# Kernel optimization log

Measured on AMD Instinct MI355X. Metric: run time of the kernel, lower is better.

The kernel has to match this reference:

```python
import jax, jax.numpy as jnp
import numpy as np

B, N, C, E = 8, 4096, 128, 131072  # batch, nodes, channels (in==out), edges


def _linear_params(key, fan_in, fan_out):
    kw, kb = jax.random.split(key)
    s = 1.0 / np.sqrt(fan_in).astype(np.float32)
    W = jax.random.uniform(kw, (fan_in, fan_out), jnp.float32, -s, s)
    b = jax.random.uniform(kb, (fan_out,), jnp.float32, -s, s)
    return W, b


def setup_inputs() -> dict:
    key = jax.random.key(0)
    ks = jax.random.split(key, 6)
    x = jax.random.normal(ks[0], (B, N, C), jnp.float32)
    edge_index = jax.random.randint(ks[1], (2, E), 0, N, jnp.int64)
    W0, b0 = _linear_params(ks[2], C, C)        # lin0: in -> out
    W1, b1 = _linear_params(ks[3], 2 * C, C)    # lin1: 2*out -> out
    W2, b2 = _linear_params(ks[4], C, C)        # lin2: out -> out
    Wo, bo = _linear_params(ks[5], C, C)        # output: out -> out
    return {"x": x, "edge_index": edge_index, "W0": W0, "b0": b0,
            "W1": W1, "b1": b1, "W2": W2, "b2": b2, "Wo": Wo, "bo": bo}


def reference(x, edge_index, W0, b0, W1, b1, W2, b2, Wo, bo):
    n = x.shape[1]
    # symmetric 0/1 adjacency (duplicate edges collapse via .set), zero diagonal
    adj = jnp.zeros((n, n), x.dtype)
    adj = adj.at[edge_index[0], edge_index[1]].set(1.0)
    adj = adj.at[edge_index[1], edge_index[0]].set(1.0)
    diag = jnp.arange(n)
    adj = adj.at[diag, diag].set(0.0)
    h = x @ W0 + b0                               # [B, N, C]
    agg = jnp.einsum('ij,bjd->bid', adj, h)       # neighbor aggregation
    cat = jnp.concatenate([x, agg], axis=-1)      # [B, N, 2C]
    out = (cat @ W1 + b1) @ W2 + b2
    out = jax.nn.gelu(out, approximate=False) @ Wo + bo  # torch exact GELU
    return x + out
```

## Files before the change

### kernel.cpp

```cpp
#include <hip/hip_runtime.h>
#include <hip/hip_bf16.h>
#include <math.h>

#define NN 4096
#define BB 8
#define CC 128
#define EE 131072
#define M_ROWS (BB*NN)
#define DEG_CAP 512

typedef __attribute__((ext_vector_type(8))) short short8;
typedef __attribute__((ext_vector_type(4))) float f32x4;

__device__ __forceinline__ float bf2f(unsigned int u){
    union { unsigned int i; float f; } v; v.i = u << 16; return v.f;
}
__device__ __forceinline__ unsigned short f2bf(float f){
    union { float f; unsigned int i; } v; v.f = f;
    unsigned int u = v.i;
    unsigned int r = u + 0x7FFFu + ((u >> 16) & 1u);
    return (unsigned short)(r >> 16);
}

__device__ __forceinline__ int swz(int r, int k2 ){
    return r * 256 + (k2 ^ ((r & 7) << 4));
}

__global__ __launch_bounds__(256) void k_init(uint4* __restrict__ bits4,
                                              const float* __restrict__ W0, const float* __restrict__ W1,
                                              const float* __restrict__ W2, const float* __restrict__ Wo,
                                              unsigned short* __restrict__ Wt0, unsigned short* __restrict__ Wt1a,
                                              unsigned short* __restrict__ Wt1b, unsigned short* __restrict__ Wt2,
                                              unsigned short* __restrict__ Wto){
    int bid = blockIdx.x, t = threadIdx.x;
    if (bid < 512){
        bits4[bid * 256 + t] = (uint4){0u, 0u, 0u, 0u};
        return;
    }
    int idx = (bid - 512) * 256 + t;
    int s = idx >> 14;
    int e = idx & 16383;
    int n = e >> 7, k = e & 127;
    float v; unsigned short* dst;
    switch (s){
        case 0:  v = W0[k*128+n];        dst = Wt0;  break;
        case 1:  v = W1[k*128+n];        dst = Wt1a; break;
        case 2:  v = W1[(128+k)*128+n];  dst = Wt1b; break;
        case 3:  v = W2[k*128+n];        dst = Wt2;  break;
        default: v = Wo[k*128+n];        dst = Wto;  break;
    }
    dst[n*128+k] = f2bf(v);
}

__global__ __launch_bounds__(256) void k_scatter(const int* __restrict__ ei,
                                                 unsigned int* __restrict__ bits){
    int e = blockIdx.x * blockDim.x + threadIdx.x;
    if (e < EE){
        int u = ei[e], v = ei[EE + e];
        atomicOr(&bits[u * 128 + (v >> 5)], 1u << (v & 31));
        atomicOr(&bits[v * 128 + (u >> 5)], 1u << (u & 31));
    }
}

__global__ __launch_bounds__(128) void k_csr(const unsigned int* __restrict__ bits,
                                             int* __restrict__ cols, int* __restrict__ deg){
    __shared__ int sc[128];
    int i = blockIdx.x, t = threadIdx.x;
    unsigned int w = bits[i * 128 + t];
    if (t == (i >> 5)) w &= ~(1u << (i & 31));
    int c = __popc(w);
    sc[t] = c; __syncthreads();
    int val = c;
    for (int off = 1; off < 128; off <<= 1){
        int add = (t >= off) ? sc[t - off] : 0;
        __syncthreads();
        val += add; sc[t] = val;
        __syncthreads();
    }
    int total = sc[127];
    int pos = val - c;
    unsigned int ww = w;
    while (ww){
        int b = __ffs(ww) - 1;
        ww &= ww - 1;
        if (pos < DEG_CAP) cols[(size_t)i * DEG_CAP + pos] = t * 32 + b;
        pos++;
    }
    if (t == 0) deg[i] = total < DEG_CAP ? total : DEG_CAP;
}

__device__ __forceinline__ void acc8u(uint4 u, float* a){
    a[0] += bf2f(u.x & 0xFFFFu); a[1] += bf2f(u.x >> 16);
    a[2] += bf2f(u.y & 0xFFFFu); a[3] += bf2f(u.y >> 16);
    a[4] += bf2f(u.z & 0xFFFFu); a[5] += bf2f(u.z >> 16);
    a[6] += bf2f(u.w & 0xFFFFu); a[7] += bf2f(u.w >> 16);
}

__global__ __launch_bounds__(256) void k_agg(const unsigned short* __restrict__ h,
                                             const int* __restrict__ cols,
                                             const int* __restrict__ deg,
                                             unsigned short* __restrict__ agg){
    __shared__ int scol[4][DEG_CAP];
    const int t = threadIdx.x;
    const int w = t >> 6, lane = t & 63;
    const int sub = lane >> 4, li = lane & 15;
    const int b = blockIdx.x & 7;
    const int i = ((blockIdx.x >> 3) << 2) + w;
    const int d = deg[i];
    const int* cl = cols + (size_t)i * DEG_CAP;
    for (int q = lane; q < d; q += 64) scol[w][q] = cl[q];

    const unsigned short* hb = h + (size_t)b * (NN*128) + li * 8;
    float a[8];
    #pragma unroll
    for (int c = 0; c < 8; c++) a[c] = 0.f;

    int n = sub;
    for (; n + 4 < d; n += 8){
        int j0 = scol[w][n], j1 = scol[w][n+4];
        uint4 u0 = *((const uint4*)(hb + ((size_t)j0 << 7)));
        uint4 u1 = *((const uint4*)(hb + ((size_t)j1 << 7)));
        acc8u(u0, a); acc8u(u1, a);
    }
    if (n < d){
        uint4 u0 = *((const uint4*)(hb + ((size_t)scol[w][n] << 7)));
        acc8u(u0, a);
    }

    #pragma unroll
    for (int c = 0; c < 8; c++){
        a[c] += __shfl_xor(a[c], 16);
        a[c] += __shfl_xor(a[c], 32);
    }
    if (sub == 0){
        uint4 o;
        o.x = (unsigned)f2bf(a[0]) | ((unsigned)f2bf(a[1]) << 16);
        o.y = (unsigned)f2bf(a[2]) | ((unsigned)f2bf(a[3]) << 16);
        o.z = (unsigned)f2bf(a[4]) | ((unsigned)f2bf(a[5]) << 16);
        o.w = (unsigned)f2bf(a[6]) | ((unsigned)f2bf(a[7]) << 16);
        *((uint4*)(agg + (size_t)b * (NN*128) + ((size_t)i << 7) + li * 8)) = o;
    }
}

__device__ __forceinline__ void stage_a_bf16(const unsigned short* __restrict__ src, int blockRow,
                                             unsigned short* As, int t){
    #pragma unroll
    for (int it = 0; it < 4; ++it){
        int g = it * 2048 + t * 8;
        int r = g >> 7, k = g & 127;
        uint4 v = *((const uint4*)(src + (size_t)(blockRow + r) * 128 + k));
        *((uint4*)((char*)As + swz(r, k * 2))) = v;
    }
}
__device__ __forceinline__ void stage_a_f32(const float* __restrict__ src, int blockRow,
                                            unsigned short* As, int t){
    #pragma unroll
    for (int it = 0; it < 4; ++it){
        int g = it * 2048 + t * 8;
        int r = g >> 7, k = g & 127;
        const float* p = src + (size_t)(blockRow + r) * 128 + k;
        float4 lo = *((const float4*)p);
        float4 hi = *((const float4*)(p + 4));
        ushort4 w0, w1;
        w0.x = f2bf(lo.x); w0.y = f2bf(lo.y); w0.z = f2bf(lo.z); w0.w = f2bf(lo.w);
        w1.x = f2bf(hi.x); w1.y = f2bf(hi.y); w1.z = f2bf(hi.z); w1.w = f2bf(hi.w);
        char* dst = (char*)As + swz(r, k * 2);
        *((ushort4*)dst) = w0;
        *((ushort4*)(dst + 8)) = w1;
    }
}
__device__ __forceinline__ void stage_w(const unsigned short* __restrict__ Wt,
                                        unsigned short* Ws, int t){
    #pragma unroll
    for (int it = 0; it < 8; ++it){
        int g = it * 2048 + t * 8;
        int r = g >> 7, k = g & 127;
        uint4 v = *((const uint4*)(Wt + r * 128 + k));
        *((uint4*)((char*)Ws + swz(r, k * 2))) = v;
    }
}
__device__ __forceinline__ void mfma_pass(const unsigned short* As, const unsigned short* Ws,
                                          int wr, int wc, int l15, int lh, f32x4 acc[2][4]){
    #pragma unroll
    for (int ks = 0; ks < 4; ++ks){
        const int kc = ks * 32 + lh * 8;
        short8 af[2], bfv[4];
        #pragma unroll
        for (int m = 0; m < 2; m++){
            int r = wr + m * 16 + l15;
            af[m] = *((const short8*)((const char*)As + swz(r, kc * 2)));
        }
        #pragma unroll
        for (int n = 0; n < 4; n++){
            int r = wc + n * 16 + l15;
            bfv[n] = *((const short8*)((const char*)Ws + swz(r, kc * 2)));
        }
        #pragma unroll
        for (int m = 0; m < 2; m++)
            #pragma unroll
            for (int n = 0; n < 4; n++)
                acc[m][n] = __builtin_amdgcn_mfma_f32_16x16x32_bf16(af[m], bfv[n], acc[m][n], 0, 0, 0);
    }
}

__global__ __launch_bounds__(256) void k_gemm0(const float* __restrict__ x,
                                               const unsigned short* __restrict__ Wt0,
                                               const float* __restrict__ b0,
                                               unsigned short* __restrict__ h){
    __shared__ unsigned short As[64*128];
    __shared__ unsigned short Ws[128*128];
    const int t = threadIdx.x;
    const int blockRow = blockIdx.x * 64;
    stage_a_f32(x, blockRow, As, t);
    stage_w(Wt0, Ws, t);
    __syncthreads();
    const int lane = t & 63, w = t >> 6;
    const int wr = (w >> 1) * 32, wc = (w & 1) * 64;
    const int l15 = lane & 15, lh = lane >> 4;
    f32x4 acc[2][4];
    #pragma unroll
    for (int m = 0; m < 2; m++) for (int n = 0; n < 4; n++) acc[m][n] = (f32x4)(0.0f);
    mfma_pass(As, Ws, wr, wc, l15, lh, acc);
    #pragma unroll
    for (int m = 0; m < 2; m++){
        #pragma unroll
        for (int rr = 0; rr < 4; rr++){
            int row = blockRow + wr + m * 16 + lh * 4 + rr;
            #pragma unroll
            for (int n = 0; n < 4; n++){
                int col = wc + n * 16 + l15;
                float v = acc[m][n][rr] + b0[col];
                h[(size_t)row * 128 + col] = f2bf(v);
            }
        }
    }
}

__global__ __launch_bounds__(256) void k_gemm1(const float* __restrict__ x,
                                               const unsigned short* __restrict__ agg,
                                               const unsigned short* __restrict__ Wt1a,
                                               const unsigned short* __restrict__ Wt1b,
                                               const float* __restrict__ b1,
                                               unsigned short* __restrict__ t1bf){
    __shared__ unsigned short As[64*128];
    __shared__ unsigned short Ws[128*128];
    const int t = threadIdx.x;
    const int blockRow = blockIdx.x * 64;
    const int lane = t & 63, w = t >> 6;
    const int wr = (w >> 1) * 32, wc = (w & 1) * 64;
    const int l15 = lane & 15, lh = lane >> 4;
    f32x4 acc[2][4];
    #pragma unroll
    for (int m = 0; m < 2; m++) for (int n = 0; n < 4; n++) acc[m][n] = (f32x4)(0.0f);

    stage_a_f32(x, blockRow, As, t);
    stage_w(Wt1a, Ws, t);
    __syncthreads();
    mfma_pass(As, Ws, wr, wc, l15, lh, acc);
    __syncthreads();
    stage_a_bf16(agg, blockRow, As, t);
    stage_w(Wt1b, Ws, t);
    __syncthreads();
    mfma_pass(As, Ws, wr, wc, l15, lh, acc);

    #pragma unroll
    for (int m = 0; m < 2; m++){
        #pragma unroll
        for (int rr = 0; rr < 4; rr++){
            int row = blockRow + wr + m * 16 + lh * 4 + rr;
            #pragma unroll
            for (int n = 0; n < 4; n++){
                int col = wc + n * 16 + l15;
                float v = acc[m][n][rr] + b1[col];
                t1bf[(size_t)row * 128 + col] = f2bf(v);
            }
        }
    }
}

__global__ __launch_bounds__(256) void k_gemm23(const unsigned short* __restrict__ t1bf,
                                                const unsigned short* __restrict__ Wt2,
                                                const unsigned short* __restrict__ Wto,
                                                const float* __restrict__ b2,
                                                const float* __restrict__ bo,
                                                const float* __restrict__ x,
                                                float* __restrict__ out){
    __shared__ unsigned short As[64*128];
    __shared__ unsigned short Ws2[128*128];
    __shared__ unsigned short Wso[128*128];
    const int t = threadIdx.x;
    const int blockRow = blockIdx.x * 64;
    const int lane = t & 63, w = t >> 6;
    const int wr = (w >> 1) * 32, wc = (w & 1) * 64;
    const int l15 = lane & 15, lh = lane >> 4;

    stage_a_bf16(t1bf, blockRow, As, t);
    stage_w(Wt2, Ws2, t);
    stage_w(Wto, Wso, t);
    __syncthreads();

    f32x4 acc[2][4];
    #pragma unroll
    for (int m = 0; m < 2; m++) for (int n = 0; n < 4; n++) acc[m][n] = (f32x4)(0.0f);
    mfma_pass(As, Ws2, wr, wc, l15, lh, acc);
    __syncthreads();

    #pragma unroll
    for (int m = 0; m < 2; m++){
        #pragma unroll
        for (int rr = 0; rr < 4; rr++){
            int rl = wr + m * 16 + lh * 4 + rr;
            #pragma unroll
            for (int n = 0; n < 4; n++){
                int col = wc + n * 16 + l15;
                float v = acc[m][n][rr] + b2[col];
                v = 0.5f * v * (1.0f + erff(v * 0.70710678118f));
                *((unsigned short*)((char*)As + swz(rl, col * 2))) = f2bf(v);
            }
        }
    }
    __syncthreads();

    f32x4 acc2[2][4];
    #pragma unroll
    for (int m = 0; m < 2; m++) for (int n = 0; n < 4; n++) acc2[m][n] = (f32x4)(0.0f);
    mfma_pass(As, Wso, wr, wc, l15, lh, acc2);

    #pragma unroll
    for (int m = 0; m < 2; m++){
        #pragma unroll
        for (int rr = 0; rr < 4; rr++){
            int row = blockRow + wr + m * 16 + lh * 4 + rr;
            #pragma unroll
            for (int n = 0; n < 4; n++){
                int col = wc + n * 16 + l15;
                float v = acc2[m][n][rr] + bo[col] + x[(size_t)row * 128 + col];
                out[(size_t)row * 128 + col] = v;
            }
        }
    }
}

extern "C" void kernel_launch(void* const* d_in, const int* in_sizes, int n_in,
                              void* d_out, int out_size, void* d_ws, size_t ws_size,
                              hipStream_t stream) {
    const float* x  = (const float*)d_in[0];
    const int*   ei = (const int*)d_in[1];
    const float* W0 = (const float*)d_in[2];
    const float* b0 = (const float*)d_in[3];
    const float* W1 = (const float*)d_in[4];
    const float* b1 = (const float*)d_in[5];
    const float* W2 = (const float*)d_in[6];
    const float* b2 = (const float*)d_in[7];
    const float* Wo = (const float*)d_in[8];
    const float* bo = (const float*)d_in[9];
    float* out = (float*)d_out;

    char* ws = (char*)d_ws;
    unsigned int* bits   = (unsigned int*)(ws + 0);
    int*   cols          = (int*)(ws + 2097152);
    int*   deg           = (int*)(ws + 10485760);
    unsigned short* h    = (unsigned short*)(ws + 10502144);
    unsigned short* aggb = (unsigned short*)(ws + 18890752);
    unsigned short* t1bf = (unsigned short*)(ws + 27279360);
    unsigned short* Wt0  = (unsigned short*)(ws + 35667968);
    unsigned short* Wt1a = (unsigned short*)(ws + 35667968 + 32768);
    unsigned short* Wt1b = (unsigned short*)(ws + 35667968 + 65536);
    unsigned short* Wt2  = (unsigned short*)(ws + 35667968 + 98304);
    unsigned short* Wto  = (unsigned short*)(ws + 35667968 + 131072);

    k_init<<<832, 256, 0, stream>>>((uint4*)bits, W0, W1, W2, Wo, Wt0, Wt1a, Wt1b, Wt2, Wto);
    k_scatter<<<EE / 256, 256, 0, stream>>>(ei, bits);
    k_csr<<<NN, 128, 0, stream>>>(bits, cols, deg);

    k_gemm0<<<M_ROWS / 64, 256, 0, stream>>>(x, Wt0, b0, h);
    k_agg<<<BB * (NN / 4), 256, 0, stream>>>(h, cols, deg, aggb);
    k_gemm1<<<M_ROWS / 64, 256, 0, stream>>>(x, aggb, Wt1a, Wt1b, b1, t1bf);
    k_gemm23<<<M_ROWS / 64, 256, 0, stream>>>(t1bf, Wt2, Wto, b2, bo, x, out);
}
```

Baseline: 77.20 us.

## Reassociate aggregation to use raw x and fold W0 into W1b; fuse MLP

Uses linearity to aggregate the bf16 copy of x directly (adj·x), then applies the precomputed product W0·W1b, and adds a degree-scaled bias term (deg·b0·W1b). This removes the separate gemm0 pass and the h intermediate. All remaining GEMMs (lin1, lin2, GELU, output) are fused into one kernel that reuses shared memory. x is converted to bf16 once in the init kernel, and a single-block kernel computes the weight product and bias vector. Risks: the serial single-block k_wprod on the critical path, and some extra precision loss from rounding the composed weight to bf16.

```diff
diff --git a/kernel.cpp b/kernel.cpp
--- a/kernel.cpp
+++ b/kernel.cpp
@@ -27,27 +27,40 @@
 }
 
 __global__ __launch_bounds__(256) void k_init(uint4* __restrict__ bits4,
+                                              const float* __restrict__ x,
+                                              unsigned short* __restrict__ xb,
                                               const float* __restrict__ W0, const float* __restrict__ W1,
                                               const float* __restrict__ W2, const float* __restrict__ Wo,
-                                              unsigned short* __restrict__ Wt0, unsigned short* __restrict__ Wt1a,
-                                              unsigned short* __restrict__ Wt1b, unsigned short* __restrict__ Wt2,
-                                              unsigned short* __restrict__ Wto){
+                                              unsigned short* __restrict__ Wt1a, unsigned short* __restrict__ Wt1b,
+                                              unsigned short* __restrict__ Wt2,  unsigned short* __restrict__ Wto,
+                                              unsigned short* __restrict__ W0bf){
     int bid = blockIdx.x, t = threadIdx.x;
     if (bid < 512){
         bits4[bid * 256 + t] = (uint4){0u, 0u, 0u, 0u};
         return;
     }
-    int idx = (bid - 512) * 256 + t;
+    if (bid < 2560){
+        size_t e = (size_t)(bid - 512) * 2048 + t * 8;
+        float4 lo = *((const float4*)(x + e));
+        float4 hi = *((const float4*)(x + e + 4));
+        ushort4 w0, w1;
+        w0.x = f2bf(lo.x); w0.y = f2bf(lo.y); w0.z = f2bf(lo.z); w0.w = f2bf(lo.w);
+        w1.x = f2bf(hi.x); w1.y = f2bf(hi.y); w1.z = f2bf(hi.z); w1.w = f2bf(hi.w);
+        *((ushort4*)(xb + e)) = w0;
+        *((ushort4*)(xb + e + 4)) = w1;
+        return;
+    }
+    int idx = (bid - 2560) * 256 + t;
     int s = idx >> 14;
     int e = idx & 16383;
     int n = e >> 7, k = e & 127;
     float v; unsigned short* dst;
     switch (s){
-        case 0:  v = W0[k*128+n];        dst = Wt0;  break;
-        case 1:  v = W1[k*128+n];        dst = Wt1a; break;
-        case 2:  v = W1[(128+k)*128+n];  dst = Wt1b; break;
-        case 3:  v = W2[k*128+n];        dst = Wt2;  break;
-        default: v = Wo[k*128+n];        dst = Wto;  break;
+        case 0:  v = W1[k*128+n];        dst = Wt1a; break;
+        case 1:  v = W1[(128+k)*128+n];  dst = Wt1b; break;
+        case 2:  v = W2[k*128+n];        dst = Wt2;  break;
+        case 3:  v = Wo[k*128+n];        dst = Wto;  break;
+        default: v = W0[n*128+k];        dst = W0bf; break;
     }
     dst[n*128+k] = f2bf(v);
 }
@@ -89,6 +102,109 @@
     if (t == 0) deg[i] = total < DEG_CAP ? total : DEG_CAP;
 }
 
+__device__ __forceinline__ void stage_w(const unsigned short* __restrict__ Wt,
+                                        unsigned short* Ws, int t){
+    #pragma unroll
+    for (int it = 0; it < 8; ++it){
+        int g = it * 2048 + t * 8;
+        int r = g >> 7, k = g & 127;
+        uint4 v = *((const uint4*)(Wt + r * 128 + k));
+        *((uint4*)((char*)Ws + swz(r, k * 2))) = v;
+    }
+}
+__device__ __forceinline__ void stage_a_bf16(const unsigned short* __restrict__ src, int blockRow,
+                                             unsigned short* As, int t){
+    #pragma unroll
+    for (int it = 0; it < 4; ++it){
+        int g = it * 2048 + t * 8;
+        int r = g >> 7, k = g & 127;
+        uint4 v = *((const uint4*)(src + (size_t)(blockRow + r) * 128 + k));
+        *((uint4*)((char*)As + swz(r, k * 2))) = v;
+    }
+}
+__device__ __forceinline__ void mfma_pass(const unsigned short* As, const unsigned short* Ws,
+                                          int wr, int wc, int l15, int lh, f32x4 acc[2][4]){
+    #pragma unroll
+    for (int ks = 0; ks < 4; ++ks){
+        const int kc = ks * 32 + lh * 8;
+        short8 af[2], bfv[4];
+        #pragma unroll
+        for (int m = 0; m < 2; m++){
+            int r = wr + m * 16 + l15;
+            af[m] = *((const short8*)((const char*)As + swz(r, kc * 2)));
+        }
+        #pragma unroll
+        for (int n = 0; n < 4; n++){
+            int r = wc + n * 16 + l15;
+            bfv[n] = *((const short8*)((const char*)Ws + swz(r, kc * 2)));
+        }
+        #pragma unroll
+        for (int m = 0; m < 2; m++)
+            #pragma unroll
+            for (int n = 0; n < 4; n++)
+                acc[m][n] = __builtin_amdgcn_mfma_f32_16x16x32_bf16(af[m], bfv[n], acc[m][n], 0, 0, 0);
+    }
+}
+
+__global__ __launch_bounds__(256) void k_wprod(const unsigned short* __restrict__ W0bf,
+                                               const unsigned short* __restrict__ Wt1b,
+                                               const float* __restrict__ b0,
+                                               const float* __restrict__ W1,
+                                               unsigned short* __restrict__ Wtu,
+                                               float* __restrict__ c1){
+    __shared__ unsigned short As[128*128];
+    __shared__ unsigned short Ws[128*128];
+    const int t = threadIdx.x;
+    stage_w(W0bf, As, t);
+    stage_w(Wt1b, Ws, t);
+    __syncthreads();
+    const int lane = t & 63, w = t >> 6;
+    const int wr = w * 32;
+    const int l15 = lane & 15, lh = lane >> 4;
+    f32x4 acc[2][8];
+    #pragma unroll
+    for (int m = 0; m < 2; m++) for (int n = 0; n < 8; n++) acc[m][n] = (f32x4)(0.0f);
+    #pragma unroll
+    for (int ks = 0; ks < 4; ++ks){
+        const int kc = ks * 32 + lh * 8;
+        short8 af[2], bfv[8];
+        #pragma unroll
+        for (int m = 0; m < 2; m++){
+            int r = wr + m * 16 + l15;
+            af[m] = *((const short8*)((const char*)As + swz(r, kc * 2)));
+        }
+        #pragma unroll
+        for (int n = 0; n < 8; n++){
+            int r = n * 16 + l15;
+            bfv[n] = *((const short8*)((const char*)Ws + swz(r, kc * 2)));
+        }
+        #pragma unroll
+        for (int m = 0; m < 2; m++)
+            #pragma unroll
+            for (int n = 0; n < 8; n++)
+                acc[m][n] = __builtin_amdgcn_mfma_f32_16x16x32_bf16(af[m], bfv[n], acc[m][n], 0, 0, 0);
+    }
+    #pragma unroll
+    for (int m = 0; m < 2; m++){
+        #pragma unroll
+        for (int rr = 0; rr < 4; rr++){
+            int r = wr + m * 16 + lh * 4 + rr;
+            #pragma unroll
+            for (int n = 0; n < 8; n++){
+                int c = n * 16 + l15;
+                Wtu[c * 128 + r] = f2bf(acc[m][n][rr]);
+            }
+        }
+    }
+    if (t < 128){
+        float s = 0.f;
+        #pragma unroll 8
+        for (int k = 0; k < 128; k++)
+            s += b0[k] * W1[(size_t)(128 + k) * 128 + t];
+        c1[t] = s;
+    }
+}
+
 __device__ __forceinline__ void acc8u(uint4 u, float* a){
     a[0] += bf2f(u.x & 0xFFFFu); a[1] += bf2f(u.x >> 16);
     a[2] += bf2f(u.y & 0xFFFFu); a[3] += bf2f(u.y >> 16);
@@ -126,7 +242,6 @@
         uint4 u0 = *((const uint4*)(hb + ((size_t)scol[w][n] << 7)));
         acc8u(u0, a);
     }
-
     #pragma unroll
     for (int c = 0; c < 8; c++){
         a[c] += __shfl_xor(a[c], 16);
@@ -142,106 +257,19 @@
     }
 }
 
-__device__ __forceinline__ void stage_a_bf16(const unsigned short* __restrict__ src, int blockRow,
-                                             unsigned short* As, int t){
-    #pragma unroll
-    for (int it = 0; it < 4; ++it){
-        int g = it * 2048 + t * 8;
-        int r = g >> 7, k = g & 127;
-        uint4 v = *((const uint4*)(src + (size_t)(blockRow + r) * 128 + k));
-        *((uint4*)((char*)As + swz(r, k * 2))) = v;
-    }
-}
-__device__ __forceinline__ void stage_a_f32(const float* __restrict__ src, int blockRow,
-                                            unsigned short* As, int t){
-    #pragma unroll
-    for (int it = 0; it < 4; ++it){
-        int g = it * 2048 + t * 8;
-        int r = g >> 7, k = g & 127;
-        const float* p = src + (size_t)(blockRow + r) * 128 + k;
-        float4 lo = *((const float4*)p);
-        float4 hi = *((const float4*)(p + 4));
-        ushort4 w0, w1;
-        w0.x = f2bf(lo.x); w0.y = f2bf(lo.y); w0.z = f2bf(lo.z); w0.w = f2bf(lo.w);
-        w1.x = f2bf(hi.x); w1.y = f2bf(hi.y); w1.z = f2bf(hi.z); w1.w = f2bf(hi.w);
-        char* dst = (char*)As + swz(r, k * 2);
-        *((ushort4*)dst) = w0;
-        *((ushort4*)(dst + 8)) = w1;
-    }
-}
-__device__ __forceinline__ void stage_w(const unsigned short* __restrict__ Wt,
-                                        unsigned short* Ws, int t){
-    #pragma unroll
-    for (int it = 0; it < 8; ++it){
-        int g = it * 2048 + t * 8;
-        int r = g >> 7, k = g & 127;
-        uint4 v = *((const uint4*)(Wt + r * 128 + k));
-        *((uint4*)((char*)Ws + swz(r, k * 2))) = v;
-    }
-}
-__device__ __forceinline__ void mfma_pass(const unsigned short* As, const unsigned short* Ws,
-                                          int wr, int wc, int l15, int lh, f32x4 acc[2][4]){
-    #pragma unroll
-    for (int ks = 0; ks < 4; ++ks){
-        const int kc = ks * 32 + lh * 8;
-        short8 af[2], bfv[4];
-        #pragma unroll
-        for (int m = 0; m < 2; m++){
-            int r = wr + m * 16 + l15;
-            af[m] = *((const short8*)((const char*)As + swz(r, kc * 2)));
-        }
-        #pragma unroll
-        for (int n = 0; n < 4; n++){
-            int r = wc + n * 16 + l15;
-            bfv[n] = *((const short8*)((const char*)Ws + swz(r, kc * 2)));
-        }
-        #pragma unroll
-        for (int m = 0; m < 2; m++)
-            #pragma unroll
-            for (int n = 0; n < 4; n++)
-                acc[m][n] = __builtin_amdgcn_mfma_f32_16x16x32_bf16(af[m], bfv[n], acc[m][n], 0, 0, 0);
-    }
-}
-
-__global__ __launch_bounds__(256) void k_gemm0(const float* __restrict__ x,
-                                               const unsigned short* __restrict__ Wt0,
-                                               const float* __restrict__ b0,
-                                               unsigned short* __restrict__ h){
-    __shared__ unsigned short As[64*128];
-    __shared__ unsigned short Ws[128*128];
-    const int t = threadIdx.x;
-    const int blockRow = blockIdx.x * 64;
-    stage_a_f32(x, blockRow, As, t);
-    stage_w(Wt0, Ws, t);
-    __syncthreads();
-    const int lane = t & 63, w = t >> 6;
-    const int wr = (w >> 1) * 32, wc = (w & 1) * 64;
-    const int l15 = lane & 15, lh = lane >> 4;
-    f32x4 acc[2][4];
-    #pragma unroll
-    for (int m = 0; m < 2; m++) for (int n = 0; n < 4; n++) acc[m][n] = (f32x4)(0.0f);
-    mfma_pass(As, Ws, wr, wc, l15, lh, acc);
-    #pragma unroll
-    for (int m = 0; m < 2; m++){
-        #pragma unroll
-        for (int rr = 0; rr < 4; rr++){
-            int row = blockRow + wr + m * 16 + lh * 4 + rr;
-            #pragma unroll
-            for (int n = 0; n < 4; n++){
-                int col = wc + n * 16 + l15;
-                float v = acc[m][n][rr] + b0[col];
-                h[(size_t)row * 128 + col] = f2bf(v);
-            }
-        }
-    }
-}
-
-__global__ __launch_bounds__(256) void k_gemm1(const float* __restrict__ x,
-                                               const unsigned short* __restrict__ agg,
-                                               const unsigned short* __restrict__ Wt1a,
-                                               const unsigned short* __restrict__ Wt1b,
-                                               const float* __restrict__ b1,
-                                               unsigned short* __restrict__ t1bf){
+__global__ __launch_bounds__(256) void k_mlp(const unsigned short* __restrict__ xb,
+                                             const unsigned short* __restrict__ u,
+                                             const unsigned short* __restrict__ Wt1a,
+                                             const unsigned short* __restrict__ Wtu,
+                                             const unsigned short* __restrict__ Wt2,
+                                             const unsigned short* __restrict__ Wto,
+                                             const float* __restrict__ c1,
+                                             const float* __restrict__ b1,
+                                             const float* __restrict__ b2,
+                                             const float* __restrict__ bo,
+                                             const int* __restrict__ deg,
+                                             const float* __restrict__ x,
+                                             float* __restrict__ out){
     __shared__ unsigned short As[64*128];
     __shared__ unsigned short Ws[128*128];
     const int t = threadIdx.x;
@@ -249,60 +277,44 @@
     const int lane = t & 63, w = t >> 6;
     const int wr = (w >> 1) * 32, wc = (w & 1) * 64;
     const int l15 = lane & 15, lh = lane >> 4;
+
     f32x4 acc[2][4];
     #pragma unroll
     for (int m = 0; m < 2; m++) for (int n = 0; n < 4; n++) acc[m][n] = (f32x4)(0.0f);
 
-    stage_a_f32(x, blockRow, As, t);
+    stage_a_bf16(xb, blockRow, As, t);
     stage_w(Wt1a, Ws, t);
     __syncthreads();
     mfma_pass(As, Ws, wr, wc, l15, lh, acc);
     __syncthreads();
-    stage_a_bf16(agg, blockRow, As, t);
-    stage_w(Wt1b, Ws, t);
+    stage_a_bf16(u, blockRow, As, t);
+    stage_w(Wtu, Ws, t);
     __syncthreads();
     mfma_pass(As, Ws, wr, wc, l15, lh, acc);
+    __syncthreads();
 
     #pragma unroll
     for (int m = 0; m < 2; m++){
         #pragma unroll
         for (int rr = 0; rr < 4; rr++){
-            int row = blockRow + wr + m * 16 + lh * 4 + rr;
+            int rl = wr + m * 16 + lh * 4 + rr;
+            int node = (blockRow + rl) & (NN - 1);
+            float degf = (float)deg[node];
             #pragma unroll
             for (int n = 0; n < 4; n++){
                 int col = wc + n * 16 + l15;
-                float v = acc[m][n][rr] + b1[col];
-                t1bf[(size_t)row * 128 + col] = f2bf(v);
+                float v = acc[m][n][rr] + b1[col] + degf * c1[col];
+                *((unsigned short*)((char*)As + swz(rl, col * 2))) = f2bf(v);
             }
         }
     }
-}
-
-__global__ __launch_bounds__(256) void k_gemm23(const unsigned short* __restrict__ t1bf,
-                                                const unsigned short* __restrict__ Wt2,
-                                                const unsigned short* __restrict__ Wto,
-                                                const float* __restrict__ b2,
-                                                const float* __restrict__ bo,
-                                                const float* __restrict__ x,
-                                                float* __restrict__ out){
-    __shared__ unsigned short As[64*128];
-    __shared__ unsigned short Ws2[128*128];
-    __shared__ unsigned short Wso[128*128];
-    const int t = threadIdx.x;
-    const int blockRow = blockIdx.x * 64;
-    const int lane = t & 63, w = t >> 6;
-    const int wr = (w >> 1) * 32, wc = (w & 1) * 64;
-    const int l15 = lane & 15, lh = lane >> 4;
-
-    stage_a_bf16(t1bf, blockRow, As, t);
-    stage_w(Wt2, Ws2, t);
-    stage_w(Wto, Wso, t);
-    __syncthreads();
-
-    f32x4 acc[2][4];
-    #pragma unroll
-    for (int m = 0; m < 2; m++) for (int n = 0; n < 4; n++) acc[m][n] = (f32x4)(0.0f);
-    mfma_pass(As, Ws2, wr, wc, l15, lh, acc);
+    stage_w(Wt2, Ws, t);
+    __syncthreads();
+
+    f32x4 acc2[2][4];
+    #pragma unroll
+    for (int m = 0; m < 2; m++) for (int n = 0; n < 4; n++) acc2[m][n] = (f32x4)(0.0f);
+    mfma_pass(As, Ws, wr, wc, l15, lh, acc2);
     __syncthreads();
 
     #pragma unroll
@@ -313,18 +325,19 @@
             #pragma unroll
             for (int n = 0; n < 4; n++){
                 int col = wc + n * 16 + l15;
-                float v = acc[m][n][rr] + b2[col];
+                float v = acc2[m][n][rr] + b2[col];
                 v = 0.5f * v * (1.0f + erff(v * 0.70710678118f));
                 *((unsigned short*)((char*)As + swz(rl, col * 2))) = f2bf(v);
             }
         }
     }
-    __syncthreads();
-
-    f32x4 acc2[2][4];
-    #pragma unroll
-    for (int m = 0; m < 2; m++) for (int n = 0; n < 4; n++) acc2[m][n] = (f32x4)(0.0f);
-    mfma_pass(As, Wso, wr, wc, l15, lh, acc2);
+    stage_w(Wto, Ws, t);
+    __syncthreads();
+
+    f32x4 acc3[2][4];
+    #pragma unroll
+    for (int m = 0; m < 2; m++) for (int n = 0; n < 4; n++) acc3[m][n] = (f32x4)(0.0f);
+    mfma_pass(As, Ws, wr, wc, l15, lh, acc3);
 
     #pragma unroll
     for (int m = 0; m < 2; m++){
@@ -334,7 +347,7 @@
             #pragma unroll
             for (int n = 0; n < 4; n++){
                 int col = wc + n * 16 + l15;
-                float v = acc2[m][n][rr] + bo[col] + x[(size_t)row * 128 + col];
+                float v = acc3[m][n][rr] + bo[col] + x[(size_t)row * 128 + col];
                 out[(size_t)row * 128 + col] = v;
             }
         }
@@ -360,21 +373,22 @@
     unsigned int* bits   = (unsigned int*)(ws + 0);
     int*   cols          = (int*)(ws + 2097152);
     int*   deg           = (int*)(ws + 10485760);
-    unsigned short* h    = (unsigned short*)(ws + 10502144);
-    unsigned short* aggb = (unsigned short*)(ws + 18890752);
-    unsigned short* t1bf = (unsigned short*)(ws + 27279360);
-    unsigned short* Wt0  = (unsigned short*)(ws + 35667968);
-    unsigned short* Wt1a = (unsigned short*)(ws + 35667968 + 32768);
-    unsigned short* Wt1b = (unsigned short*)(ws + 35667968 + 65536);
-    unsigned short* Wt2  = (unsigned short*)(ws + 35667968 + 98304);
-    unsigned short* Wto  = (unsigned short*)(ws + 35667968 + 131072);
-
-    k_init<<<832, 256, 0, stream>>>((uint4*)bits, W0, W1, W2, Wo, Wt0, Wt1a, Wt1b, Wt2, Wto);
+    unsigned short* xb   = (unsigned short*)(ws + 10502144);
+    unsigned short* ubuf = (unsigned short*)(ws + 18890752);
+    unsigned short* Wt1a = (unsigned short*)(ws + 27279360);
+    unsigned short* Wt1b = (unsigned short*)(ws + 27279360 + 32768);
+    unsigned short* Wt2  = (unsigned short*)(ws + 27279360 + 65536);
+    unsigned short* Wto  = (unsigned short*)(ws + 27279360 + 98304);
+    unsigned short* W0bf = (unsigned short*)(ws + 27279360 + 131072);
+    unsigned short* Wtu  = (unsigned short*)(ws + 27279360 + 163840);
+    float* c1            = (float*)(ws + 27279360 + 196608);
+
+    k_init<<<2880, 256, 0, stream>>>((uint4*)bits, x, xb, W0, W1, W2, Wo,
+                                     Wt1a, Wt1b, Wt2, Wto, W0bf);
     k_scatter<<<EE / 256, 256, 0, stream>>>(ei, bits);
     k_csr<<<NN, 128, 0, stream>>>(bits, cols, deg);
-
-    k_gemm0<<<M_ROWS / 64, 256, 0, stream>>>(x, Wt0, b0, h);
-    k_agg<<<BB * (NN / 4), 256, 0, stream>>>(h, cols, deg, aggb);
-    k_gemm1<<<M_ROWS / 64, 256, 0, stream>>>(x, aggb, Wt1a, Wt1b, b1, t1bf);
-    k_gemm23<<<M_ROWS / 64, 256, 0, stream>>>(t1bf, Wt2, Wto, b2, bo, x, out);
-}
+    k_wprod<<<1, 256, 0, stream>>>(W0bf, Wt1b, b0, W1, Wtu, c1);
+    k_agg<<<BB * (NN / 4), 256, 0, stream>>>(xb, cols, deg, ubuf);
+    k_mlp<<<M_ROWS / 64, 256, 0, stream>>>(xb, ubuf, Wt1a, Wtu, Wt2, Wto,
+                                           c1, b1, b2, bo, deg, x, out);
+}
```

After: 77.13 us. No clear change (-0.1%).
